# Kernel tuning notes

Hardware: AMD Instinct MI355X
Metric: run time of the kernel (lower is better)

## Reference

```python
import jax, jax.numpy as jnp
import numpy as np

K = 1024  # number of superpixel ids (matches fill_max of superpixel)

@jax.custom_vjp
def smooth_square(x):
    return x * x

def _ss_fwd(x):
    return x * x, x

def _ss_bwd(x, g):
    # gradient of square with input clipped to [-1, 1]
    return (g * 2.0 * jnp.clip(x, -1.0, 1.0),)

smooth_square.defvjp(_ss_fwd, _ss_bwd)

def setup_inputs() -> dict:
    key = jax.random.key(0)
    k1, k2 = jax.random.split(key)
    D, H, W = 64, 1024, 1024
    embedding = jax.random.normal(k1, (D, H, W), dtype=jnp.float32)
    superpixel = jax.random.randint(k2, (H, W), 0, K, dtype=jnp.int64)
    return {"embedding": embedding, "superpixel": superpixel}

def reference(embedding, superpixel):
    # embedding: D x H x W float, superpixel: H x W int
    D = embedding.shape[0]
    sp = superpixel.reshape(-1)                      # N = H*W
    x = embedding.reshape(D, -1)                     # D x N
    ones = jnp.ones(sp.shape, dtype=x.dtype)
    counts = jax.ops.segment_sum(ones, sp, num_segments=K)        # K
    sums = jax.ops.segment_sum(x.T, sp, num_segments=K)           # K x D
    mean = sums / jnp.maximum(counts, 1.0)[:, None]                # K x D
    dev = x - mean[sp].T                              # D x N, scores - per-segment mean
    # sum over all segments of D*variance*count == sum of squared deviations
    return smooth_square(dev).sum()
```

## Files before the change

### kernel.cpp

```cpp
#include <hip/hip_runtime.h>
#include <stdint.h>

#define K_SEG 1024
#define D_CH 64
#define CHUNK 32768
#define ABLK 512
#define PREP_B 128


__global__ void __launch_bounds__(256)
prep_kernel(const int* __restrict__ spw, uint16_t* __restrict__ sp16,
            uint32_t* __restrict__ cnt_part, float* __restrict__ sums,
            uint32_t* __restrict__ ticket, int N) {
    __shared__ uint32_t h[4][K_SEG];
    __shared__ int wideflag;
    const int t = threadIdx.x;
    const int b = blockIdx.x;
    {
        uint32_t* hf = &h[0][0];
        for (int i = t; i < 4 * K_SEG; i += 256) hf[i] = 0u;
    }
    if (t < 64) {
        int odd = spw[2 * t + 1];
        unsigned long long bal = __ballot(odd == 0);
        if (t == 0) wideflag = (bal == ~0ULL) ? 1 : 0;
    }
    if (b == 0 && t == 0) *ticket = 0u;
    if (b < D_CH)
        for (int i = t; i < K_SEG; i += 256) sums[b * K_SEG + i] = 0.0f;
    __syncthreads();
    const bool wide = (wideflag != 0);
    uint32_t* ht = h[t >> 6];
    const int stride = PREP_B * 256;
    #pragma unroll 4
    for (int n = b * 256 + t; n < N; n += stride) {
        int v = wide ? spw[2 * n] : spw[n];
        v &= (K_SEG - 1);
        sp16[n] = (uint16_t)v;
        ht[v] += 1u;
    }
    __syncthreads();
    for (int k = t; k < K_SEG; k += 256)
        cnt_part[b * K_SEG + k] = h[0][k] + h[1][k] + h[2][k] + h[3][k];
}

__global__ void __launch_bounds__(ABLK, 8)
accum_kernel(const float* __restrict__ emb, const uint16_t* __restrict__ sp16,
             float* __restrict__ sums, double* __restrict__ xsq_part, int N) {
    __shared__ float2 lsum[4][K_SEG];
    __shared__ float wsum[8];
    const int t = threadIdx.x;
    float2* tile = lsum[(t >> 6) & 3];
    {
        float2* lf = &lsum[0][0];
        for (int i = t; i < 4 * K_SEG; i += ABLK) lf[i] = make_float2(0.0f, 0.0f);
    }
    __syncthreads();

    const int g = blockIdx.x;
    const int c = blockIdx.y;
    const int base = c * CHUNK;
    const float* e0 = emb + (size_t)(2 * g) * N + base;
    const float* e1 = e0 + N;
    const uint16_t* sp = sp16 + base;
    float acc = 0.0f;
    const int NIT = CHUNK / (ABLK * 4);

    if (base + CHUNK <= N) {
        int q = t * 4;
        ushort4 k4 = *reinterpret_cast<const ushort4*>(sp + q);
        float4 v0 = *reinterpret_cast<const float4*>(e0 + q);
        float4 v1 = *reinterpret_cast<const float4*>(e1 + q);
        #pragma unroll 2
        for (int it = 0; it < NIT; ++it) {
            const int qn = q + ABLK * 4;
            ushort4 k4n = k4; float4 v0n = v0, v1n = v1;
            if (it + 1 < NIT) {
                k4n = *reinterpret_cast<const ushort4*>(sp + qn);
                v0n = *reinterpret_cast<const float4*>(e0 + qn);
                v1n = *reinterpret_cast<const float4*>(e1 + qn);
            }
            acc += v0.x * v0.x + v0.y * v0.y + v0.z * v0.z + v0.w * v0.w;
            acc += v1.x * v1.x + v1.y * v1.y + v1.z * v1.z + v1.w * v1.w;
            float2 o0 = tile[k4.x];
            float2 o1 = tile[k4.y];
            float2 o2 = tile[k4.z];
            float2 o3 = tile[k4.w];
            o0.x += v0.x; o0.y += v1.x;
            o1.x += v0.y; o1.y += v1.y;
            o2.x += v0.z; o2.y += v1.z;
            o3.x += v0.w; o3.y += v1.w;
            tile[k4.x] = o0;
            tile[k4.y] = o1;
            tile[k4.z] = o2;
            tile[k4.w] = o3;
            q = qn; k4 = k4n; v0 = v0n; v1 = v1n;
        }
    } else {
        for (int it = 0; it < NIT; ++it) {
            const int p = base + it * ABLK * 4 + t * 4;
            if (p + 4 <= N) {
                const ushort4 k4 = *reinterpret_cast<const ushort4*>(sp16 + p);
                const float4 v0 = *reinterpret_cast<const float4*>(emb + (size_t)(2 * g) * N + p);
                const float4 v1 = *reinterpret_cast<const float4*>(emb + (size_t)(2 * g + 1) * N + p);
                acc += v0.x * v0.x + v0.y * v0.y + v0.z * v0.z + v0.w * v0.w;
                acc += v1.x * v1.x + v1.y * v1.y + v1.z * v1.z + v1.w * v1.w;
                float2 o0 = tile[k4.x], o1 = tile[k4.y], o2 = tile[k4.z], o3 = tile[k4.w];
                o0.x += v0.x; o0.y += v1.x;
                o1.x += v0.y; o1.y += v1.y;
                o2.x += v0.z; o2.y += v1.z;
                o3.x += v0.w; o3.y += v1.w;
                tile[k4.x] = o0; tile[k4.y] = o1; tile[k4.z] = o2; tile[k4.w] = o3;
            }
        }
    }
    __syncthreads();

    for (int k = t; k < K_SEG; k += ABLK) {
        float2 s0 = lsum[0][k], s1 = lsum[1][k], s2 = lsum[2][k], s3 = lsum[3][k];
        atomicAdd(&sums[(size_t)(2 * g) * K_SEG + k], s0.x + s1.x + s2.x + s3.x);
        atomicAdd(&sums[(size_t)(2 * g + 1) * K_SEG + k], s0.y + s1.y + s2.y + s3.y);
    }

    #pragma unroll
    for (int off = 32; off; off >>= 1) acc += __shfl_down(acc, off, 64);
    if ((t & 63) == 0) wsum[t >> 6] = acc;
    __syncthreads();
    if (t == 0) {
        double bsum = 0.0;
        #pragma unroll
        for (int w = 0; w < 8; ++w) bsum += (double)wsum[w];
        xsq_part[c * gridDim.x + g] = bsum;
    }
}

__global__ void __launch_bounds__(256)
finalize_kernel(const float* __restrict__ sums, const uint32_t* __restrict__ cnt_part,
                const double* __restrict__ xsq_part, double* __restrict__ term_part,
                uint32_t* __restrict__ ticket, float* __restrict__ out,
                int n_xsq) {
    const int t = threadIdx.x;
    const int b = blockIdx.x;
    const int k0 = b * 16;
    __shared__ float cinv[16];
    if (t < 16) {
        uint32_t c = 0;
        #pragma unroll 8
        for (int p = 0; p < PREP_B; ++p) c += cnt_part[p * K_SEG + k0 + t];
        cinv[t] = 1.0f / fmaxf((float)c, 1.0f);
    }
    __syncthreads();
    double acc = 0.0;
    for (int e = t; e < D_CH * 16; e += 256) {
        const int d = e >> 4, kk = e & 15;
        const float s = sums[d * K_SEG + k0 + kk];
        acc += (double)(s * s) * (double)cinv[kk];
    }
    __shared__ double sacc[256];
    sacc[t] = acc;
    __syncthreads();
    for (int off = 128; off; off >>= 1) {
        if (t < off) sacc[t] += sacc[t + off];
        __syncthreads();
    }
    __shared__ int last;
    if (t == 0) {
        term_part[b] = sacc[0];
        __threadfence();
        last = (atomicAdd(ticket, 1u) == gridDim.x - 1) ? 1 : 0;
    }
    __syncthreads();
    if (last) {
        double a = 0.0;
        for (int i = t; i < n_xsq; i += 256) a += xsq_part[i];
        if (t < 64) a -= atomicAdd(&term_part[t], 0.0);
        sacc[t] = a;
        __syncthreads();
        for (int off = 128; off; off >>= 1) {
            if (t < off) sacc[t] += sacc[t + off];
            __syncthreads();
        }
        if (t == 0) out[0] = (float)sacc[0];
    }
}

extern "C" void kernel_launch(void* const* d_in, const int* in_sizes, int n_in,
                              void* d_out, int out_size, void* d_ws, size_t ws_size,
                              hipStream_t stream) {
    const float* emb = (const float*)d_in[0];
    const int* spw = (const int*)d_in[1];
    const int N = in_sizes[1];

    char* ws = (char*)d_ws;
    uint32_t* ticket = (uint32_t*)(ws + 0);
    double* term_part = (double*)(ws + 64);
    double* xsq_part = (double*)(ws + 1024);
    float* sums = (float*)(ws + 16384);
    uint32_t* cnt_part = (uint32_t*)(ws + 278528);
    uint16_t* sp16 = (uint16_t*)(ws + 802816);

    prep_kernel<<<PREP_B, 256, 0, stream>>>(spw, sp16, cnt_part, sums, ticket, N);

    dim3 grid(D_CH / 2, (N + CHUNK - 1) / CHUNK);
    accum_kernel<<<grid, ABLK, 0, stream>>>(emb, sp16, sums, xsq_part, N);

    const int n_xsq = grid.x * grid.y;
    finalize_kernel<<<64, 256, 0, stream>>>(sums, cnt_part, xsq_part, term_part,
                                            ticket, (float*)d_out, n_xsq);
}
```

Baseline: 68.12 us.

## Double sums buffer to split atomics, deepen prefetch, double prep blocks

Three changes at once. The sums accumulator is split into two copies chosen by chunk parity, which halves atomic contention on each address, and finalize adds the two copies back together. The accumulate loop now prefetches two iterations ahead instead of one, at the cost of extra registers. The prep kernel goes from 128 to 256 blocks and clears both sums copies, which doubles the partial count arrays finalize must reduce; workspace offsets are moved to fit.

```diff
diff --git a/kernel.cpp b/kernel.cpp
--- a/kernel.cpp
+++ b/kernel.cpp
@@ -5,7 +5,7 @@
 #define D_CH 64
 #define CHUNK 32768
 #define ABLK 512
-#define PREP_B 128
+#define PREP_B 256
 
 
 __global__ void __launch_bounds__(256)
@@ -26,8 +26,8 @@
         if (t == 0) wideflag = (bal == ~0ULL) ? 1 : 0;
     }
     if (b == 0 && t == 0) *ticket = 0u;
-    if (b < D_CH)
-        for (int i = t; i < K_SEG; i += 256) sums[b * K_SEG + i] = 0.0f;
+    for (int i = t; i < (2 * D_CH * K_SEG) / PREP_B; i += 256)
+        sums[b * ((2 * D_CH * K_SEG) / PREP_B) + i] = 0.0f;
     __syncthreads();
     const bool wide = (wideflag != 0);
     uint32_t* ht = h[t >> 6];
@@ -41,7 +41,7 @@
     }
     __syncthreads();
     for (int k = t; k < K_SEG; k += 256)
-        cnt_part[b * K_SEG + k] = h[0][k] + h[1][k] + h[2][k] + h[3][k];
+        cnt_part[(size_t)b * K_SEG + k] = h[0][k] + h[1][k] + h[2][k] + h[3][k];
 }
 
 __global__ void __launch_bounds__(ABLK, 8)
@@ -67,34 +67,40 @@
     const int NIT = CHUNK / (ABLK * 4);
 
     if (base + CHUNK <= N) {
-        int q = t * 4;
-        ushort4 k4 = *reinterpret_cast<const ushort4*>(sp + q);
-        float4 v0 = *reinterpret_cast<const float4*>(e0 + q);
-        float4 v1 = *reinterpret_cast<const float4*>(e1 + q);
+        int q0 = t * 4;
+        ushort4 ka = *reinterpret_cast<const ushort4*>(sp + q0);
+        float4 va0 = *reinterpret_cast<const float4*>(e0 + q0);
+        float4 va1 = *reinterpret_cast<const float4*>(e1 + q0);
+        int q1 = q0 + ABLK * 4;
+        ushort4 kb = *reinterpret_cast<const ushort4*>(sp + q1);
+        float4 vb0 = *reinterpret_cast<const float4*>(e0 + q1);
+        float4 vb1 = *reinterpret_cast<const float4*>(e1 + q1);
         #pragma unroll 2
         for (int it = 0; it < NIT; ++it) {
-            const int qn = q + ABLK * 4;
-            ushort4 k4n = k4; float4 v0n = v0, v1n = v1;
-            if (it + 1 < NIT) {
-                k4n = *reinterpret_cast<const ushort4*>(sp + qn);
-                v0n = *reinterpret_cast<const float4*>(e0 + qn);
-                v1n = *reinterpret_cast<const float4*>(e1 + qn);
+            ushort4 kc = kb; float4 vc0 = vb0, vc1 = vb1;
+            if (it + 2 < NIT) {
+                const int q2 = q0 + 2 * ABLK * 4;
+                kc = *reinterpret_cast<const ushort4*>(sp + q2);
+                vc0 = *reinterpret_cast<const float4*>(e0 + q2);
+                vc1 = *reinterpret_cast<const float4*>(e1 + q2);
             }
-            acc += v0.x * v0.x + v0.y * v0.y + v0.z * v0.z + v0.w * v0.w;
-            acc += v1.x * v1.x + v1.y * v1.y + v1.z * v1.z + v1.w * v1.w;
-            float2 o0 = tile[k4.x];
-            float2 o1 = tile[k4.y];
-            float2 o2 = tile[k4.z];
-            float2 o3 = tile[k4.w];
-            o0.x += v0.x; o0.y += v1.x;
-            o1.x += v0.y; o1.y += v1.y;
-            o2.x += v0.z; o2.y += v1.z;
-            o3.x += v0.w; o3.y += v1.w;
-            tile[k4.x] = o0;
-            tile[k4.y] = o1;
-            tile[k4.z] = o2;
-            tile[k4.w] = o3;
-            q = qn; k4 = k4n; v0 = v0n; v1 = v1n;
+            acc += va0.x * va0.x + va0.y * va0.y + va0.z * va0.z + va0.w * va0.w;
+            acc += va1.x * va1.x + va1.y * va1.y + va1.z * va1.z + va1.w * va1.w;
+            float2 o0 = tile[ka.x];
+            float2 o1 = tile[ka.y];
+            float2 o2 = tile[ka.z];
+            float2 o3 = tile[ka.w];
+            o0.x += va0.x; o0.y += va1.x;
+            o1.x += va0.y; o1.y += va1.y;
+            o2.x += va0.z; o2.y += va1.z;
+            o3.x += va0.w; o3.y += va1.w;
+            tile[ka.x] = o0;
+            tile[ka.y] = o1;
+            tile[ka.z] = o2;
+            tile[ka.w] = o3;
+            q0 += ABLK * 4;
+            ka = kb; va0 = vb0; va1 = vb1;
+            kb = kc; vb0 = vc0; vb1 = vc1;
         }
     } else {
         for (int it = 0; it < NIT; ++it) {
@@ -116,10 +122,11 @@
     }
     __syncthreads();
 
+    float* dst = sums + (size_t)(c & 1) * (D_CH * K_SEG);
     for (int k = t; k < K_SEG; k += ABLK) {
         float2 s0 = lsum[0][k], s1 = lsum[1][k], s2 = lsum[2][k], s3 = lsum[3][k];
-        atomicAdd(&sums[(size_t)(2 * g) * K_SEG + k], s0.x + s1.x + s2.x + s3.x);
-        atomicAdd(&sums[(size_t)(2 * g + 1) * K_SEG + k], s0.y + s1.y + s2.y + s3.y);
+        atomicAdd(&dst[(size_t)(2 * g) * K_SEG + k], s0.x + s1.x + s2.x + s3.x);
+        atomicAdd(&dst[(size_t)(2 * g + 1) * K_SEG + k], s0.y + s1.y + s2.y + s3.y);
     }
 
     #pragma unroll
@@ -146,14 +153,15 @@
     if (t < 16) {
         uint32_t c = 0;
         #pragma unroll 8
-        for (int p = 0; p < PREP_B; ++p) c += cnt_part[p * K_SEG + k0 + t];
+        for (int p = 0; p < PREP_B; ++p) c += cnt_part[(size_t)p * K_SEG + k0 + t];
         cinv[t] = 1.0f / fmaxf((float)c, 1.0f);
     }
     __syncthreads();
     double acc = 0.0;
     for (int e = t; e < D_CH * 16; e += 256) {
         const int d = e >> 4, kk = e & 15;
-        const float s = sums[d * K_SEG + k0 + kk];
+        const float s = sums[d * K_SEG + k0 + kk] +
+                        sums[D_CH * K_SEG + d * K_SEG + k0 + kk];
         acc += (double)(s * s) * (double)cinv[kk];
     }
     __shared__ double sacc[256];
@@ -196,8 +204,8 @@
     double* term_part = (double*)(ws + 64);
     double* xsq_part = (double*)(ws + 1024);
     float* sums = (float*)(ws + 16384);
-    uint32_t* cnt_part = (uint32_t*)(ws + 278528);
-    uint16_t* sp16 = (uint16_t*)(ws + 802816);
+    uint32_t* cnt_part = (uint32_t*)(ws + 540672);
+    uint16_t* sp16 = (uint16_t*)(ws + 1589248);
 
     prep_kernel<<<PREP_B, 256, 0, stream>>>(spw, sp16, cnt_part, sums, ticket, N);
 
```

Result: no change. 69.05 us (+1.4%).
